# Kernel tuning notes

Hardware: AMD Instinct MI355X
Metric: run time of the kernel (lower is better)

The kernel has to match this reference:

```python
import jax, jax.numpy as jnp
import numpy as np

NUM_SLOTS = 4096
NUM_CLUSTER = 10
SLOT_DIM = 64
EPS = 1e-8
N_ITER = 3
LN_EPS = 1e-5


def _ln(x, g, b):
    m = jnp.mean(x, axis=-1, keepdims=True)
    v = jnp.var(x, axis=-1, keepdims=True)
    return (x - m) / jnp.sqrt(v + LN_EPS) * g + b


def setup_inputs() -> dict:
    key = jax.random.key(0)
    ks = jax.random.split(key, 24)
    d, S = SLOT_DIM, NUM_SLOTS
    s = d ** -0.5
    f32 = jnp.float32
    return {
        "cluster_centers": jax.random.normal(ks[0], (NUM_CLUSTER, d), f32),
        "Wk": jax.random.normal(ks[1], (d, d), f32) * s,
        "bk": jnp.zeros((d,), f32),
        "Wq": jax.random.normal(ks[2], (d, d), f32) * s,
        "bq": jnp.zeros((d,), f32),
        "Wv": jax.random.normal(ks[3], (d, d), f32) * s,
        "bv": jnp.zeros((d,), f32),
        "cc_g": jnp.ones((d,), f32),
        "cc_b": jnp.zeros((d,), f32),
        "W_ih": jax.random.normal(ks[4], (3 * d, d), f32) * s,
        "W_hh": jax.random.normal(ks[5], (3 * d, d), f32) * s,
        "b_ih": jnp.zeros((3 * d,), f32),
        "b_hh": jnp.zeros((3 * d,), f32),
        "ln_g": jnp.ones((d,), f32),
        "ln_b": jnp.zeros((d,), f32),
        "W1": jax.random.normal(ks[6], (2 * d, d), f32) * s,
        "b1": jnp.zeros((2 * d,), f32),
        "W2": jax.random.normal(ks[7], (d, 2 * d), f32) * (2 * d) ** -0.5,
        "b2": jnp.zeros((d,), f32),
        "Wa": jax.random.normal(ks[8], (S, d, d), f32) * s,
        "ba": jnp.zeros((S, d), f32),
        "Wb": jax.random.normal(ks[9], (S, d, d), f32) * s,
        "bb": jnp.zeros((S, d), f32),
    }


def reference(cluster_centers, Wk, bk, Wq, bq, Wv, bv, cc_g, cc_b,
              W_ih, W_hh, b_ih, b_hh, ln_g, ln_b, W1, b1, W2, b2,
              Wa, ba, Wb, bb):
    temp = SLOT_DIM ** -0.5
    k = cluster_centers @ Wk.T + bk          # [N, d]
    v = cluster_centers @ Wv.T + bv          # [N, d]
    cc = cluster_centers
    for _ in range(N_ITER):
        cc_prev = cc
        q = _ln(cc, cc_g, cc_b) @ Wq.T + bq  # [N, d]
        attn = jnp.einsum('nd,md->nm', k, q) * temp
        attn = jax.nn.softmax(attn, axis=0) + EPS
        attn = attn / jnp.sum(attn, axis=-1, keepdims=True)
        updates = attn @ v                   # [N, d]
        # PyTorch GRUCell
        gi = updates @ W_ih.T + b_ih
        gh = cc_prev @ W_hh.T + b_hh
        ir, iz, inn = jnp.split(gi, 3, axis=-1)
        hr, hz, hn = jnp.split(gh, 3, axis=-1)
        r = jax.nn.sigmoid(ir + hr)
        z = jax.nn.sigmoid(iz + hz)
        n = jnp.tanh(inn + r * hn)
        cc = (1.0 - z) * n + z * cc_prev
        # residual MLP
        h = _ln(cc, ln_g, ln_b)
        cc = cc + jax.nn.relu(h @ W1.T + b1) @ W2.T + b2
    # per-slot 2-layer MLP + max over the 10 clusters, vectorized over slots
    h = jax.nn.relu(jnp.einsum('sij,nj->sni', Wa, cc) + ba[:, None, :])  # [S, N, d]
    out = jnp.einsum('sij,snj->sni', Wb, h) + bb[:, None, :]             # [S, N, d]
    return jnp.max(out, axis=1)                                          # [S, d]
```

## Files before the change

kernel.cpp:

```cpp
#include <hip/hip_runtime.h>
#include <math.h>

#define NCLU 10
#define D    64
#define NSLOT 4096

typedef unsigned int   u32;
typedef unsigned short u16;

typedef __attribute__((ext_vector_type(8))) short  bf16x8;
typedef __attribute__((ext_vector_type(4))) float  f32x4;

__device__ __forceinline__ u16 f2bf_rne(float f) {
    u32 u = __float_as_uint(f);
    return (u16)((u + 0x7fffu + ((u >> 16) & 1u)) >> 16);
}

__device__ __forceinline__ bf16x8 pack8(float4 a, float4 b) {
    bf16x8 r;
    r[0] = (short)f2bf_rne(a.x); r[1] = (short)f2bf_rne(a.y);
    r[2] = (short)f2bf_rne(a.z); r[3] = (short)f2bf_rne(a.w);
    r[4] = (short)f2bf_rne(b.x); r[5] = (short)f2bf_rne(b.y);
    r[6] = (short)f2bf_rne(b.z); r[7] = (short)f2bf_rne(b.w);
    return r;
}

__device__ __forceinline__ float wred(float v) {
#pragma unroll
    for (int off = 32; off > 0; off >>= 1) v += __shfl_xor(v, off);
    return v;
}

__device__ __forceinline__ void load_afrags64(bf16x8 a[4][2], const float* __restrict__ W,
                                              int lc, int quad) {
#pragma unroll
    for (int mt = 0; mt < 4; ++mt)
#pragma unroll
        for (int kt = 0; kt < 2; ++kt) {
            const float* p = W + (16 * mt + lc) * 64 + kt * 32 + quad * 8;
            a[mt][kt] = pack8(*(const float4*)p, *(const float4*)(p + 4));
        }
}

__device__ __forceinline__ void load_afrags128(bf16x8 a[4][2], const float* __restrict__ W,
                                               int ktbase, int lc, int quad) {
#pragma unroll
    for (int mt = 0; mt < 4; ++mt)
#pragma unroll
        for (int kt = 0; kt < 2; ++kt) {
            const float* p = W + (16 * mt + lc) * 128 + (ktbase + kt) * 32 + quad * 8;
            a[mt][kt] = pack8(*(const float4*)p, *(const float4*)(p + 4));
        }
}

__device__ __forceinline__ bf16x8 bfrag(const float* __restrict__ xbase, int xstride,
                                        int lc, int quad, int ktglob) {
    if (lc < NCLU) {
        const float* p = xbase + lc * xstride + ktglob * 32 + quad * 8;
        return pack8(*(const float4*)p, *(const float4*)(p + 4));
    }
    bf16x8 z;
#pragma unroll
    for (int j = 0; j < 8; ++j) z[j] = 0;
    return z;
}

__device__ __forceinline__ void mm_apply(const bf16x8 a[4][2], const float* __restrict__ xbase,
                                         int xstride, int ktbase,
                                         float* __restrict__ obase, int ostride, int ooff,
                                         const float4 bp[4], bool use_bias, bool do_relu,
                                         int lc, int quad) {
    f32x4 acc[4];
#pragma unroll
    for (int mt = 0; mt < 4; ++mt) acc[mt] = (f32x4){0.f, 0.f, 0.f, 0.f};
#pragma unroll
    for (int kt = 0; kt < 2; ++kt) {
        bf16x8 b = bfrag(xbase, xstride, lc, quad, ktbase + kt);
#pragma unroll
        for (int mt = 0; mt < 4; ++mt)
            acc[mt] = __builtin_amdgcn_mfma_f32_16x16x32_bf16(a[mt][kt], b, acc[mt], 0, 0, 0);
    }
    if (lc < NCLU) {
#pragma unroll
        for (int mt = 0; mt < 4; ++mt) {
            float4 o;
            o.x = acc[mt][0]; o.y = acc[mt][1]; o.z = acc[mt][2]; o.w = acc[mt][3];
            if (use_bias) {
                o.x += bp[mt].x; o.y += bp[mt].y; o.z += bp[mt].z; o.w += bp[mt].w;
            }
            if (do_relu) {
                o.x = fmaxf(o.x, 0.f); o.y = fmaxf(o.y, 0.f);
                o.z = fmaxf(o.z, 0.f); o.w = fmaxf(o.w, 0.f);
            }
            *(float4*)(obase + lc * ostride + ooff + 16 * mt + 4 * quad) = o;
        }
    }
}

__global__ __launch_bounds__(640, 3) void phase1_kernel(
    const float* __restrict__ cc0,
    const float* __restrict__ Wk, const float* __restrict__ bk,
    const float* __restrict__ Wq, const float* __restrict__ bq,
    const float* __restrict__ Wv, const float* __restrict__ bv,
    const float* __restrict__ cc_g, const float* __restrict__ cc_b,
    const float* __restrict__ W_ih, const float* __restrict__ W_hh,
    const float* __restrict__ b_ih, const float* __restrict__ b_hh,
    const float* __restrict__ ln_g, const float* __restrict__ ln_b,
    const float* __restrict__ W1, const float* __restrict__ b1,
    const float* __restrict__ W2, const float* __restrict__ b2,
    float* __restrict__ cc_out)
{
    const int t = threadIdx.x;
    const int w = t >> 6;
    const int i = t & 63;
    const int quad = i >> 4;
    const int lc   = i & 15;

    __shared__ float ccl[NCLU][68];
    __shared__ float xl[NCLU][68];
    __shared__ float kl[NCLU][68];
    __shared__ float vl[NCLU][68];
    __shared__ float ql[NCLU][68];
    __shared__ float ul[NCLU][68];
    __shared__ float hl[NCLU][68];
    __shared__ float dl9[NCLU][68];
    __shared__ float dl8[NCLU][68];
    __shared__ float tl[NCLU][132];
    __shared__ float gl[6][NCLU][68];
    __shared__ float al[NCLU][12];

    const float g_cc = cc_g[i], b_cc = cc_b[i];
    const float g_ln = ln_g[i], b_ln = ln_b[i];

    bf16x8 afrA[4][2], afrB[4][2];
#pragma unroll
    for (int mt = 0; mt < 4; ++mt)
#pragma unroll
        for (int kt = 0; kt < 2; ++kt) {
#pragma unroll
            for (int j = 0; j < 8; ++j) { afrA[mt][kt][j] = 0; afrB[mt][kt][j] = 0; }
        }

    const float* biasA = nullptr;
    if (w == 0)      { load_afrags64(afrA, Wq, lc, quad);                       biasA = bq; }
    else if (w <= 3) { load_afrags64(afrA, W_ih + (w - 1) * 64 * 64, lc, quad); biasA = b_ih + (w - 1) * 64; }
    else if (w <= 6) { load_afrags64(afrA, W_hh + (w - 4) * 64 * 64, lc, quad); biasA = b_hh + (w - 4) * 64; }
    else if (w == 7) { load_afrags64(afrA, Wk, lc, quad);                       biasA = bk; }
    else if (w == 8) { load_afrags64(afrA, Wv, lc, quad);                       biasA = bv;
                       load_afrags128(afrB, W2, 2, lc, quad); }
    else             { load_afrags128(afrA, W2, 0, lc, quad);                   biasA = b2; }

    float4 bpre[4];
#pragma unroll
    for (int mt = 0; mt < 4; ++mt) { bpre[mt].x = bpre[mt].y = bpre[mt].z = bpre[mt].w = 0.f; }
    if (biasA) {
#pragma unroll
        for (int mt = 0; mt < 4; ++mt) bpre[mt] = *(const float4*)(biasA + 16 * mt + 4 * quad);
    }

    float c = cc0[w * 64 + i];
    ccl[w][i] = c;
    __syncthreads();

    if (w == 7)      mm_apply(afrA, &ccl[0][0], 68, 0, &kl[0][0], 68, 0, bpre, true, false, lc, quad);
    else if (w == 8) mm_apply(afrA, &ccl[0][0], 68, 0, &vl[0][0], 68, 0, bpre, true, false, lc, quad);
    __syncthreads();

    if (w == 7) {
        load_afrags64(afrA, W1, lc, quad);
#pragma unroll
        for (int mt = 0; mt < 4; ++mt) bpre[mt] = *(const float4*)(b1 + 16 * mt + 4 * quad);
    } else if (w == 8) {
        load_afrags64(afrA, W1 + 64 * 64, lc, quad);
#pragma unroll
        for (int mt = 0; mt < 4; ++mt) bpre[mt] = *(const float4*)(b1 + 64 + 16 * mt + 4 * quad);
    }

    for (int it = 0; it < 3; ++it) {
        {
            float s1 = wred(c), s2 = wred(c * c);
            float mu = s1 * (1.f / 64.f);
            float va = s2 * (1.f / 64.f) - mu * mu;
            xl[w][i] = (c - mu) * rsqrtf(va + 1e-5f) * g_cc + b_cc;
        }
        __syncthreads();

        if (w == 0)
            mm_apply(afrA, &xl[0][0], 68, 0, &ql[0][0], 68, 0, bpre, true, false, lc, quad);
        else if (w >= 4 && w <= 6)
            mm_apply(afrA, &ccl[0][0], 68, 0, &gl[w - 1][0][0], 68, 0, bpre, true, false, lc, quad);
        __syncthreads();

        if (i < NCLU) {
            const float4* kf = (const float4*)&kl[w][0];
            const float4* qf = (const float4*)&ql[i][0];
            float a0 = 0.f, a1 = 0.f, a2 = 0.f, a3 = 0.f;
#pragma unroll
            for (int jj = 0; jj < 16; ++jj) {
                float4 kv = kf[jj], qv = qf[jj];
                a0 += kv.x * qv.x; a1 += kv.y * qv.y; a2 += kv.z * qv.z; a3 += kv.w * qv.w;
            }
            al[w][i] = ((a0 + a1) + (a2 + a3)) * 0.125f;
        }
        __syncthreads();

        {
            float e[NCLU];
            if (i < NCLU) {
                float mx = -1e30f;
#pragma unroll
                for (int nn = 0; nn < NCLU; ++nn) mx = fmaxf(mx, al[nn][i]);
                float s = 0.f;
#pragma unroll
                for (int nn = 0; nn < NCLU; ++nn) { e[nn] = __expf(al[nn][i] - mx); s += e[nn]; }
                float inv = 1.f / s;
#pragma unroll
                for (int nn = 0; nn < NCLU; ++nn) e[nn] = e[nn] * inv + 1e-8f;
            } else {
#pragma unroll
                for (int nn = 0; nn < NCLU; ++nn) e[nn] = 0.f;
            }
            float rs[NCLU];
#pragma unroll
            for (int nn = 0; nn < NCLU; ++nn) rs[nn] = e[nn];
#pragma unroll
            for (int off = 1; off < 16; off <<= 1) {
#pragma unroll
                for (int nn = 0; nn < NCLU; ++nn) rs[nn] += __shfl_xor(rs[nn], off);
            }
            float ew = 0.f, rw = 1.f;
#pragma unroll
            for (int nn = 0; nn < NCLU; ++nn) if (nn == w) { ew = e[nn]; rw = rs[nn]; }
            float val = (i < NCLU) ? ew / rw : 0.f;
            float u = 0.f;
#pragma unroll
            for (int m = 0; m < NCLU; ++m) u += __shfl(val, m) * vl[m][i];
            ul[w][i] = u;
        }
        __syncthreads();

        if (w >= 1 && w <= 3)
            mm_apply(afrA, &ul[0][0], 68, 0, &gl[w - 1][0][0], 68, 0, bpre, true, false, lc, quad);
        __syncthreads();

        {
            float ir = gl[0][w][i], iz = gl[1][w][i], inn = gl[2][w][i];
            float hr = gl[3][w][i], hz = gl[4][w][i], hn = gl[5][w][i];
            float r = 1.f / (1.f + __expf(-(ir + hr)));
            float z = 1.f / (1.f + __expf(-(iz + hz)));
            float xt = inn + r * hn;
            float ex2 = __expf(2.f * xt);
            float nn2 = 1.f - 2.f / (ex2 + 1.f);
            c = (1.f - z) * nn2 + z * c;

            float s1 = wred(c), s2 = wred(c * c);
            float mu = s1 * (1.f / 64.f);
            float va = s2 * (1.f / 64.f) - mu * mu;
            hl[w][i] = (c - mu) * rsqrtf(va + 1e-5f) * g_ln + b_ln;
        }
        __syncthreads();

        if (w == 7)
            mm_apply(afrA, &hl[0][0], 68, 0, &tl[0][0], 132, 0, bpre, true, true, lc, quad);
        else if (w == 8)
            mm_apply(afrA, &hl[0][0], 68, 0, &tl[0][0], 132, 64, bpre, true, true, lc, quad);
        __syncthreads();

        if (w == 9)
            mm_apply(afrA, &tl[0][0], 132, 0, &dl9[0][0], 68, 0, bpre, true, false, lc, quad);
        else if (w == 8)
            mm_apply(afrB, &tl[0][0], 132, 2, &dl8[0][0], 68, 0, bpre, false, false, lc, quad);
        __syncthreads();

        c += dl9[w][i] + dl8[w][i];
        ccl[w][i] = c;
    }

    cc_out[w * 64 + i] = c;
}

#define HSTR 72
__global__ __launch_bounds__(256, 5) void phase2_kernel(
    const float* __restrict__ Wa, const float* __restrict__ ba,
    const float* __restrict__ Wb, const float* __restrict__ bb,
    const float* __restrict__ cc, float* __restrict__ out)
{
    const int w = threadIdx.x >> 6;
    const int l = threadIdx.x & 63;
    const int s = blockIdx.x;
    const int quad = l >> 4;
    const int lc   = l & 15;

    __shared__ u16 hT[16 * HSTR];

    const float* wa = Wa + (size_t)s * 4096;
    const float* wb = Wb + (size_t)s * 4096;

    float4 c00, c01, c10, c11;
    if (lc < NCLU) {
        const float* cp = cc + lc * 64;
        c00 = *(const float4*)(cp + 0 * 32 + quad * 8);
        c01 = *(const float4*)(cp + 0 * 32 + quad * 8 + 4);
        c10 = *(const float4*)(cp + 1 * 32 + quad * 8);
        c11 = *(const float4*)(cp + 1 * 32 + quad * 8 + 4);
    }
    float4 a00, a01, a10, a11;
    {
        const float* p0 = wa + (16 * w + lc) * 64 + 0 * 32 + quad * 8;
        const float* p1 = wa + (16 * w + lc) * 64 + 1 * 32 + quad * 8;
        a00 = *(const float4*)p0; a01 = *(const float4*)(p0 + 4);
        a10 = *(const float4*)p1; a11 = *(const float4*)(p1 + 4);
    }
    float4 bav = *(const float4*)(ba + s * 64 + 16 * w + quad * 4);
    float4 b00, b01, b10, b11;
    {
        const float* p0 = wb + (16 * w + lc) * 64 + 0 * 32 + quad * 8;
        const float* p1 = wb + (16 * w + lc) * 64 + 1 * 32 + quad * 8;
        b00 = *(const float4*)p0; b01 = *(const float4*)(p0 + 4);
        b10 = *(const float4*)p1; b11 = *(const float4*)(p1 + 4);
    }

    bf16x8 frA[2];
    frA[0] = pack8(a00, a01);
    frA[1] = pack8(a10, a11);
    bf16x8 bcc[2];
    if (lc < NCLU) {
        bcc[0] = pack8(c00, c01);
        bcc[1] = pack8(c10, c11);
    } else {
#pragma unroll
        for (int j = 0; j < 8; ++j) { bcc[0][j] = 0; bcc[1][j] = 0; }
    }

    f32x4 acc = (f32x4){0.f, 0.f, 0.f, 0.f};
    acc = __builtin_amdgcn_mfma_f32_16x16x32_bf16(frA[0], bcc[0], acc, 0, 0, 0);
    acc = __builtin_amdgcn_mfma_f32_16x16x32_bf16(frA[1], bcc[1], acc, 0, 0, 0);

    {
        u16 h0 = f2bf_rne(fmaxf(acc[0] + bav.x, 0.f));
        u16 h1 = f2bf_rne(fmaxf(acc[1] + bav.y, 0.f));
        u16 h2 = f2bf_rne(fmaxf(acc[2] + bav.z, 0.f));
        u16 h3 = f2bf_rne(fmaxf(acc[3] + bav.w, 0.f));
        uint2 pk; pk.x = (u32)h0 | ((u32)h1 << 16); pk.y = (u32)h2 | ((u32)h3 << 16);
        *(uint2*)(&hT[lc * HSTR + 16 * w + quad * 4]) = pk;
    }

    bf16x8 frB[2];
    frB[0] = pack8(b00, b01);
    frB[1] = pack8(b10, b11);

    __syncthreads();

    bf16x8 bh[2];
#pragma unroll
    for (int kt = 0; kt < 2; ++kt)
        bh[kt] = *(const bf16x8*)(&hT[lc * HSTR + kt * 32 + quad * 8]);

    f32x4 acc2 = (f32x4){0.f, 0.f, 0.f, 0.f};
    acc2 = __builtin_amdgcn_mfma_f32_16x16x32_bf16(frB[0], bh[0], acc2, 0, 0, 0);
    acc2 = __builtin_amdgcn_mfma_f32_16x16x32_bf16(frB[1], bh[1], acc2, 0, 0, 0);

    const float NEG = -3.0e38f;
#pragma unroll
    for (int r = 0; r < 4; ++r) {
        float v = (lc < NCLU) ? acc2[r] : NEG;
#pragma unroll
        for (int off = 1; off < 16; off <<= 1)
            v = fmaxf(v, __shfl_xor(v, off));
        acc2[r] = v;
    }

    if (lc < 4) {
        int row = 16 * w + 4 * quad + lc;
        out[s * 64 + row] = acc2[lc] + bb[s * 64 + row];
    }
}

extern "C" void kernel_launch(void* const* d_in, const int* in_sizes, int n_in,
                              void* d_out, int out_size, void* d_ws, size_t ws_size,
                              hipStream_t stream) {
    const float* cc0  = (const float*)d_in[0];
    const float* Wk   = (const float*)d_in[1];
    const float* bk   = (const float*)d_in[2];
    const float* Wq   = (const float*)d_in[3];
    const float* bq   = (const float*)d_in[4];
    const float* Wv   = (const float*)d_in[5];
    const float* bv   = (const float*)d_in[6];
    const float* ccg  = (const float*)d_in[7];
    const float* ccb  = (const float*)d_in[8];
    const float* Wih  = (const float*)d_in[9];
    const float* Whh  = (const float*)d_in[10];
    const float* bih  = (const float*)d_in[11];
    const float* bhh  = (const float*)d_in[12];
    const float* lng  = (const float*)d_in[13];
    const float* lnb  = (const float*)d_in[14];
    const float* W1   = (const float*)d_in[15];
    const float* b1   = (const float*)d_in[16];
    const float* W2   = (const float*)d_in[17];
    const float* b2   = (const float*)d_in[18];
    const float* Wa   = (const float*)d_in[19];
    const float* ba   = (const float*)d_in[20];
    const float* Wb   = (const float*)d_in[21];
    const float* bb   = (const float*)d_in[22];

    float* cc_ws = (float*)d_ws;
    float* out   = (float*)d_out;

    hipLaunchKernelGGL(phase1_kernel, dim3(1), dim3(640), 0, stream,
                       cc0, Wk, bk, Wq, bq, Wv, bv, ccg, ccb,
                       Wih, Whh, bih, bhh, lng, lnb, W1, b1, W2, b2, cc_ws);

    hipLaunchKernelGGL(phase2_kernel, dim3(NSLOT), dim3(256), 0, stream,
                       Wa, ba, Wb, bb, cc_ws, out);
}
```

Before: 222.9 us.

## Process four slots per block with double-buffered register prefetch in phase2

```diff
diff --git a/kernel.cpp b/kernel.cpp
--- a/kernel.cpp
+++ b/kernel.cpp
@@ -280,21 +280,19 @@
 }
 
 #define HSTR 72
-__global__ __launch_bounds__(256, 5) void phase2_kernel(
+#define SLOTS_PER_BLK 4
+__global__ __launch_bounds__(256, 4) void phase2_kernel(
     const float* __restrict__ Wa, const float* __restrict__ ba,
     const float* __restrict__ Wb, const float* __restrict__ bb,
     const float* __restrict__ cc, float* __restrict__ out)
 {
     const int w = threadIdx.x >> 6;
     const int l = threadIdx.x & 63;
-    const int s = blockIdx.x;
     const int quad = l >> 4;
     const int lc   = l & 15;
-
-    __shared__ u16 hT[16 * HSTR];
-
-    const float* wa = Wa + (size_t)s * 4096;
-    const float* wb = Wb + (size_t)s * 4096;
+    const int s0 = blockIdx.x * SLOTS_PER_BLK;
+
+    __shared__ u16 hT[2][16 * HSTR];
 
     float4 c00, c01, c10, c11;
     if (lc < NCLU) {
@@ -304,25 +302,34 @@
         c10 = *(const float4*)(cp + 1 * 32 + quad * 8);
         c11 = *(const float4*)(cp + 1 * 32 + quad * 8 + 4);
     }
-    float4 a00, a01, a10, a11;
-    {
-        const float* p0 = wa + (16 * w + lc) * 64 + 0 * 32 + quad * 8;
-        const float* p1 = wa + (16 * w + lc) * 64 + 1 * 32 + quad * 8;
-        a00 = *(const float4*)p0; a01 = *(const float4*)(p0 + 4);
-        a10 = *(const float4*)p1; a11 = *(const float4*)(p1 + 4);
-    }
-    float4 bav = *(const float4*)(ba + s * 64 + 16 * w + quad * 4);
-    float4 b00, b01, b10, b11;
-    {
-        const float* p0 = wb + (16 * w + lc) * 64 + 0 * 32 + quad * 8;
-        const float* p1 = wb + (16 * w + lc) * 64 + 1 * 32 + quad * 8;
-        b00 = *(const float4*)p0; b01 = *(const float4*)(p0 + 4);
-        b10 = *(const float4*)p1; b11 = *(const float4*)(p1 + 4);
-    }
-
-    bf16x8 frA[2];
-    frA[0] = pack8(a00, a01);
-    frA[1] = pack8(a10, a11);
+
+    float bbs[SLOTS_PER_BLK];
+    if (lc < 4) {
+#pragma unroll
+        for (int j = 0; j < SLOTS_PER_BLK; ++j)
+            bbs[j] = bb[(s0 + j) * 64 + 16 * w + 4 * quad + lc];
+    }
+
+    float4 rA[2][4], rB[2][4];
+    float4 bav[2];
+
+    auto ISSUE = [&](int j, int bank) {
+        const int s = s0 + j;
+        const float* wa = Wa + (size_t)s * 4096 + (16 * w + lc) * 64 + quad * 8;
+        const float* wb = Wb + (size_t)s * 4096 + (16 * w + lc) * 64 + quad * 8;
+        rA[bank][0] = *(const float4*)(wa);
+        rA[bank][1] = *(const float4*)(wa + 4);
+        rA[bank][2] = *(const float4*)(wa + 32);
+        rA[bank][3] = *(const float4*)(wa + 36);
+        rB[bank][0] = *(const float4*)(wb);
+        rB[bank][1] = *(const float4*)(wb + 4);
+        rB[bank][2] = *(const float4*)(wb + 32);
+        rB[bank][3] = *(const float4*)(wb + 36);
+        bav[bank] = *(const float4*)(ba + s * 64 + 16 * w + quad * 4);
+    };
+
+    ISSUE(0, 0);
+
     bf16x8 bcc[2];
     if (lc < NCLU) {
         bcc[0] = pack8(c00, c01);
@@ -332,47 +339,55 @@
         for (int j = 0; j < 8; ++j) { bcc[0][j] = 0; bcc[1][j] = 0; }
     }
 
-    f32x4 acc = (f32x4){0.f, 0.f, 0.f, 0.f};
-    acc = __builtin_amdgcn_mfma_f32_16x16x32_bf16(frA[0], bcc[0], acc, 0, 0, 0);
-    acc = __builtin_amdgcn_mfma_f32_16x16x32_bf16(frA[1], bcc[1], acc, 0, 0, 0);
-
-    {
-        u16 h0 = f2bf_rne(fmaxf(acc[0] + bav.x, 0.f));
-        u16 h1 = f2bf_rne(fmaxf(acc[1] + bav.y, 0.f));
-        u16 h2 = f2bf_rne(fmaxf(acc[2] + bav.z, 0.f));
-        u16 h3 = f2bf_rne(fmaxf(acc[3] + bav.w, 0.f));
-        uint2 pk; pk.x = (u32)h0 | ((u32)h1 << 16); pk.y = (u32)h2 | ((u32)h3 << 16);
-        *(uint2*)(&hT[lc * HSTR + 16 * w + quad * 4]) = pk;
-    }
-
-    bf16x8 frB[2];
-    frB[0] = pack8(b00, b01);
-    frB[1] = pack8(b10, b11);
-
-    __syncthreads();
-
-    bf16x8 bh[2];
-#pragma unroll
-    for (int kt = 0; kt < 2; ++kt)
-        bh[kt] = *(const bf16x8*)(&hT[lc * HSTR + kt * 32 + quad * 8]);
-
-    f32x4 acc2 = (f32x4){0.f, 0.f, 0.f, 0.f};
-    acc2 = __builtin_amdgcn_mfma_f32_16x16x32_bf16(frB[0], bh[0], acc2, 0, 0, 0);
-    acc2 = __builtin_amdgcn_mfma_f32_16x16x32_bf16(frB[1], bh[1], acc2, 0, 0, 0);
-
-    const float NEG = -3.0e38f;
-#pragma unroll
-    for (int r = 0; r < 4; ++r) {
-        float v = (lc < NCLU) ? acc2[r] : NEG;
-#pragma unroll
-        for (int off = 1; off < 16; off <<= 1)
-            v = fmaxf(v, __shfl_xor(v, off));
-        acc2[r] = v;
-    }
-
-    if (lc < 4) {
-        int row = 16 * w + 4 * quad + lc;
-        out[s * 64 + row] = acc2[lc] + bb[s * 64 + row];
+#pragma unroll
+    for (int j = 0; j < SLOTS_PER_BLK; ++j) {
+        const int cur = j & 1;
+        if (j + 1 < SLOTS_PER_BLK) ISSUE(j + 1, (j + 1) & 1);
+
+        bf16x8 frA[2], frB[2];
+        frA[0] = pack8(rA[cur][0], rA[cur][1]);
+        frA[1] = pack8(rA[cur][2], rA[cur][3]);
+        frB[0] = pack8(rB[cur][0], rB[cur][1]);
+        frB[1] = pack8(rB[cur][2], rB[cur][3]);
+
+        f32x4 acc = (f32x4){0.f, 0.f, 0.f, 0.f};
+        acc = __builtin_amdgcn_mfma_f32_16x16x32_bf16(frA[0], bcc[0], acc, 0, 0, 0);
+        acc = __builtin_amdgcn_mfma_f32_16x16x32_bf16(frA[1], bcc[1], acc, 0, 0, 0);
+
+        {
+            u16 h0 = f2bf_rne(fmaxf(acc[0] + bav[cur].x, 0.f));
+            u16 h1 = f2bf_rne(fmaxf(acc[1] + bav[cur].y, 0.f));
+            u16 h2 = f2bf_rne(fmaxf(acc[2] + bav[cur].z, 0.f));
+            u16 h3 = f2bf_rne(fmaxf(acc[3] + bav[cur].w, 0.f));
+            uint2 pk; pk.x = (u32)h0 | ((u32)h1 << 16); pk.y = (u32)h2 | ((u32)h3 << 16);
+            *(uint2*)(&hT[cur][lc * HSTR + 16 * w + quad * 4]) = pk;
+        }
+
+        __syncthreads();
+
+        bf16x8 bh[2];
+#pragma unroll
+        for (int kt = 0; kt < 2; ++kt)
+            bh[kt] = *(const bf16x8*)(&hT[cur][lc * HSTR + kt * 32 + quad * 8]);
+
+        f32x4 acc2 = (f32x4){0.f, 0.f, 0.f, 0.f};
+        acc2 = __builtin_amdgcn_mfma_f32_16x16x32_bf16(frB[0], bh[0], acc2, 0, 0, 0);
+        acc2 = __builtin_amdgcn_mfma_f32_16x16x32_bf16(frB[1], bh[1], acc2, 0, 0, 0);
+
+        const float NEG = -3.0e38f;
+#pragma unroll
+        for (int r = 0; r < 4; ++r) {
+            float v = (lc < NCLU) ? acc2[r] : NEG;
+#pragma unroll
+            for (int off = 1; off < 16; off <<= 1)
+                v = fmaxf(v, __shfl_xor(v, off));
+            acc2[r] = v;
+        }
+
+        if (lc < 4) {
+            int row = 16 * w + 4 * quad + lc;
+            out[(s0 + j) * 64 + row] = acc2[lc] + bbs[j];
+        }
     }
 }
 
@@ -410,6 +425,6 @@
                        cc0, Wk, bk, Wq, bq, Wv, bv, ccg, ccb,
                        Wih, Whh, bih, bhh, lng, lnb, W1, b1, W2, b2, cc_ws);
 
-    hipLaunchKernelGGL(phase2_kernel, dim3(NSLOT), dim3(256), 0, stream,
+    hipLaunchKernelGGL(phase2_kernel, dim3(NSLOT / SLOTS_PER_BLK), dim3(256), 0, stream,
                        Wa, ba, Wb, bb, cc_ws, out);
 }
```

Result: no change. 220.6 us (-1.0%).
